# Performance work log

Hardware: AMD Instinct MI355X
Metric: run time of the kernel (lower is better)

Reference implementation:

```python
import jax, jax.numpy as jnp
import numpy as np

B, N, DN, DT = 1024, 200, 128, 128
M = DN + DN + DT  # model_dim = 384 (node + edge + time dims)


def setup_inputs() -> dict:
    key = jax.random.key(0)
    ks = jax.random.split(key, 10)
    rn = lambda k, s, sc=1.0: jax.random.normal(k, s, jnp.float32) * sc
    return {
        'src': rn(ks[0], (B, DN)),
        'src_t': rn(ks[1], (B, 1, DT)),
        'seq': rn(ks[2], (B, N, DN)),
        'seq_t': rn(ks[3], (B, N, DT)),
        'seq_e': rn(ks[4], (B, N, DN)),
        'mask': jax.random.randint(ks[5], (B, N), 0, 2).astype(bool),
        'shared_attn': rn(ks[6], (1, 2 * M), 0.05),
        'fc_w': rn(ks[7], (M, M), 0.05),
        'ln_g': jnp.ones((M,), jnp.float32),
        'ln_b': jnp.zeros((M,), jnp.float32),
        'agg_fc_w1': rn(ks[8], (2 * DN, M + DN), 0.05),
        'agg_fc_w2': rn(ks[9], (DN, 2 * DN), 0.05),
    }


def _layer_norm(x, g, b, eps=1e-5):
    mu = x.mean(-1, keepdims=True)
    var = ((x - mu) ** 2).mean(-1, keepdims=True)
    return (x - mu) * jax.lax.rsqrt(var + eps) * g + b


def reference(src, src_t, seq, seq_t, seq_e, mask, shared_attn, fc_w, ln_g, ln_b, agg_fc_w1, agg_fc_w2):
    # AttnModel.forward with 'simple' Attention (eval mode: dropout off)
    src_ext = src[:, None, :]                                   # [B,1,DN]
    q = jnp.concatenate([src_ext, jnp.zeros_like(src_ext), src_t], axis=2)  # [B,1,M]
    k = jnp.concatenate([seq, seq_e, seq_t], axis=2)            # [B,N,M]
    # F.linear(cat([q_exp, k_exp], -1), shared_attn) == q.w_q + k.w_k (fused, avoids [B,1,N,2M])
    w = shared_attn[0]
    wq, wk = w[:M], w[M:]
    scores = jnp.einsum('bqd,d->bq', q, wq)[:, :, None] + jnp.einsum('bnd,d->bn', k, wk)[:, None, :]  # [B,1,N]
    scores = jnp.where(mask[:, None, :], -1e10, scores)
    attn = jax.nn.softmax(scores, axis=2)                       # [B,1,N]
    out = jnp.einsum('bqn,bnm->bqm', attn, k)                   # [B,1,M] (v == k)
    out = out @ fc_w.T
    out = _layer_norm(out + q, ln_g, ln_b)
    out = out[:, 0, :]                                          # [B,M]
    attn_w = attn[:, 0, :]                                      # [B,N]
    x = jnp.concatenate([out, src], axis=1)                     # [B, M+DN]
    x = jax.nn.relu(x @ agg_fc_w1.T)                            # [B, 2*DN]
    out = x @ agg_fc_w2.T                                       # [B, DN]
    return out, attn_w
```

## Files before the change

### kernel.cpp

```cpp
#include <hip/hip_runtime.h>


constexpr int B_  = 1024;
constexpr int N_  = 200;
constexpr int DN_ = 128;
constexpr int DT_ = 128;
constexpr int M_  = 384;
constexpr int BDIM = 256;
constexpr int NPW  = N_ / 4;

__device__ __forceinline__ float wave_sum(float v) {
#pragma unroll
    for (int off = 32; off > 0; off >>= 1)
        v += __shfl_xor(v, off, 64);
    return v;
}

__global__ __launch_bounds__(BDIM) void tgnn_kernel(
    const float* __restrict__ src,
    const float* __restrict__ src_t,
    const float* __restrict__ seq,
    const float* __restrict__ seq_t,
    const float* __restrict__ seq_e,
    const int*   __restrict__ mask,
    const float* __restrict__ shared_attn,
    const float* __restrict__ fc_w,
    const float* __restrict__ ln_g,
    const float* __restrict__ ln_b,
    const float* __restrict__ w1,
    const float* __restrict__ w2,
    float* __restrict__ out,
    float* __restrict__ attn_out)
{
    const int b    = blockIdx.x;
    const int tid  = threadIdx.x;
    const int wave = tid >> 6;
    const int lane = tid & 63;
    const int e0   = 2 * lane;
    const int e1   = e0 + 1;

    __shared__ float s_p[N_];
    __shared__ float s_q[M_];
    __shared__ float s_oa[4][M_];
    __shared__ float s_outattn[M_];
    __shared__ float s_y[M_ + DN_];
    __shared__ float s_h[2 * DN_];
    __shared__ float s_red[8];

    if (tid < 128) {
        s_q[tid]       = src[b * DN_ + tid];
        s_q[128 + tid] = 0.0f;
        s_q[256 + tid] = src_t[b * DT_ + tid];
    }

    const float* wq = shared_attn;
    const float* wk = shared_attn + M_;
    const float wk0 = wk[e0],       wk1 = wk[e1];
    const float wk2 = wk[128 + e0], wk3 = wk[128 + e1];
    const float wk4 = wk[256 + e0], wk5 = wk[256 + e1];

    float qpart = src[b * DN_ + e0] * wq[e0]
                + src[b * DN_ + e1] * wq[e1]
                + src_t[b * DT_ + e0] * wq[256 + e0]
                + src_t[b * DT_ + e1] * wq[256 + e1];
    const float qdot = wave_sum(qpart);

    float o0 = 0.f, o1 = 0.f, o2 = 0.f, o3 = 0.f, o4 = 0.f, o5 = 0.f;
    float lsum = 0.f;
    const int n_base = wave * NPW;
    for (int n = n_base; n < n_base + NPW; ++n) {
        const long row = (long)(b * N_ + n);
        const float2 a = *(const float2*)&seq  [row * DN_ + e0];
        const float2 e = *(const float2*)&seq_e[row * DN_ + e0];
        const float2 t = *(const float2*)&seq_t[row * DT_ + e0];
        float part = a.x * wk0 + a.y * wk1
                   + e.x * wk2 + e.y * wk3
                   + t.x * wk4 + t.y * wk5;
        float s = wave_sum(part) + qdot;
        float p = mask[row] ? 0.0f : __expf(s);
        if (lane == 0) s_p[n] = p;
        lsum += p;
        o0 += p * a.x; o1 += p * a.y;
        o2 += p * e.x; o3 += p * e.y;
        o4 += p * t.x; o5 += p * t.y;
    }

    if (lane == 0) s_red[wave] = lsum;
    s_oa[wave][e0]       = o0; s_oa[wave][e1]       = o1;
    s_oa[wave][128 + e0] = o2; s_oa[wave][128 + e1] = o3;
    s_oa[wave][256 + e0] = o4; s_oa[wave][256 + e1] = o5;
    __syncthreads();

    const float Z    = s_red[0] + s_red[1] + s_red[2] + s_red[3];
    const float invZ = 1.0f / Z;

    for (int j = tid; j < M_; j += BDIM)
        s_outattn[j] = (s_oa[0][j] + s_oa[1][j] + s_oa[2][j] + s_oa[3][j]) * invZ;
    for (int n = tid; n < N_; n += BDIM)
        attn_out[b * N_ + n] = s_p[n] * invZ;
    __syncthreads();

    for (int r = 0; r < M_ / 4; ++r) {
        const int i = wave * (M_ / 4) + r;
        const float* row = &fc_w[i * M_];
        float part = 0.f;
#pragma unroll
        for (int m = 0; m < 6; ++m)
            part += s_outattn[lane + 64 * m] * row[lane + 64 * m];
        float v = wave_sum(part);
        if (lane == 0) s_y[i] = v + s_q[i];
    }
    __syncthreads();

    float ls = 0.f, lq = 0.f;
    for (int j = tid; j < M_; j += BDIM) {
        float v = s_y[j];
        ls += v; lq += v * v;
    }
    ls = wave_sum(ls); lq = wave_sum(lq);
    if (lane == 0) { s_red[wave] = ls; s_red[4 + wave] = lq; }
    __syncthreads();
    const float mean = (s_red[0] + s_red[1] + s_red[2] + s_red[3]) * (1.0f / M_);
    const float msq  = (s_red[4] + s_red[5] + s_red[6] + s_red[7]) * (1.0f / M_);
    const float rstd = rsqrtf(msq - mean * mean + 1e-5f);
    for (int j = tid; j < M_; j += BDIM)
        s_y[j] = (s_y[j] - mean) * rstd * ln_g[j] + ln_b[j];
    if (tid < 128)
        s_y[M_ + tid] = s_q[tid];
    __syncthreads();

    for (int r = 0; r < 64; ++r) {
        const int i = wave * 64 + r;
        const float* row = &w1[i * (M_ + DN_)];
        float part = 0.f;
#pragma unroll
        for (int m = 0; m < 8; ++m)
            part += s_y[lane + 64 * m] * row[lane + 64 * m];
        float v = wave_sum(part);
        if (lane == 0) s_h[i] = fmaxf(v, 0.0f);
    }
    __syncthreads();

    for (int r = 0; r < 32; ++r) {
        const int i = wave * 32 + r;
        const float* row = &w2[i * (2 * DN_)];
        float part = 0.f;
#pragma unroll
        for (int m = 0; m < 4; ++m)
            part += s_h[lane + 64 * m] * row[lane + 64 * m];
        float v = wave_sum(part);
        if (lane == 0) out[b * DN_ + i] = v;
    }
}

extern "C" void kernel_launch(void* const* d_in, const int* in_sizes, int n_in,
                              void* d_out, int out_size, void* d_ws, size_t ws_size,
                              hipStream_t stream) {
    const float* src         = (const float*)d_in[0];
    const float* src_t       = (const float*)d_in[1];
    const float* seq         = (const float*)d_in[2];
    const float* seq_t       = (const float*)d_in[3];
    const float* seq_e       = (const float*)d_in[4];
    const int*   mask        = (const int*)  d_in[5];
    const float* shared_attn = (const float*)d_in[6];
    const float* fc_w        = (const float*)d_in[7];
    const float* ln_g        = (const float*)d_in[8];
    const float* ln_b        = (const float*)d_in[9];
    const float* w1          = (const float*)d_in[10];
    const float* w2          = (const float*)d_in[11];

    float* out      = (float*)d_out;
    float* attn_out = (float*)d_out + B_ * DN_;

    tgnn_kernel<<<B_, BDIM, 0, stream>>>(src, src_t, seq, seq_t, seq_e, mask,
                                         shared_attn, fc_w, ln_g, ln_b, w1, w2,
                                         out, attn_out);
}
```

Before: 424.0 us.

## Process two batch rows per block, pre-transpose weights, and prefetch keys

A separate kernel now transposes fc_w, w1 and w2 into global buffers each call, so each thread computes one output column with coalesced weight reads instead of one row per wave followed by a shuffle reduction. The main kernel handles two batch rows per 512-thread block, which reuses every weight load across both rows. The key loop moves to float4 loads, with half-waves each handling one key row, and software-prefetches two iterations ahead. The mask is staged in shared memory. The cost is an extra transpose launch per call, higher register pressure and shared-memory use, and half as many blocks.

```diff
diff --git a/kernel.cpp b/kernel.cpp
--- a/kernel.cpp
+++ b/kernel.cpp
@@ -1,22 +1,53 @@
 #include <hip/hip_runtime.h>
 
 
-constexpr int B_  = 1024;
-constexpr int N_  = 200;
-constexpr int DN_ = 128;
-constexpr int DT_ = 128;
-constexpr int M_  = 384;
-constexpr int BDIM = 256;
-constexpr int NPW  = N_ / 4;
-
+constexpr int B_   = 1024;
+constexpr int N_   = 200;
+constexpr int DN_  = 128;
+constexpr int DT_  = 128;
+constexpr int M_   = 384;
+constexpr int BDIM = 512;
+constexpr int ROWS = 2;
+constexpr int WPR  = 4;
+constexpr int NPW  = N_ / WPR;
+constexpr int PAIRS = NPW / 2;
+
+__device__ float g_fcT[M_ * M_];
+__device__ float g_w1T[(M_ + DN_) * (2 * DN_)];
+__device__ float g_w2T[(2 * DN_) * DN_];
+
+__device__ __forceinline__ float half_sum(float v) {
+#pragma unroll
+    for (int off = 16; off > 0; off >>= 1) v += __shfl_xor(v, off, 64);
+    return v;
+}
 __device__ __forceinline__ float wave_sum(float v) {
 #pragma unroll
-    for (int off = 32; off > 0; off >>= 1)
-        v += __shfl_xor(v, off, 64);
+    for (int off = 32; off > 0; off >>= 1) v += __shfl_xor(v, off, 64);
     return v;
 }
 
-__global__ __launch_bounds__(BDIM) void tgnn_kernel(
+struct KP { float4 a, e, t; };
+
+__global__ void transpose_weights(const float* __restrict__ fc_w,
+                                  const float* __restrict__ w1,
+                                  const float* __restrict__ w2) {
+    const int stride = gridDim.x * blockDim.x;
+    for (int idx = blockIdx.x * blockDim.x + threadIdx.x; idx < M_ * M_; idx += stride) {
+        const int j = idx / M_, i = idx - j * M_;
+        g_fcT[idx] = fc_w[i * M_ + j];
+    }
+    for (int idx = blockIdx.x * blockDim.x + threadIdx.x; idx < (M_ + DN_) * (2 * DN_); idx += stride) {
+        const int j = idx >> 8, i = idx & 255;
+        g_w1T[idx] = w1[i * (M_ + DN_) + j];
+    }
+    for (int idx = blockIdx.x * blockDim.x + threadIdx.x; idx < (2 * DN_) * DN_; idx += stride) {
+        const int j = idx >> 7, i = idx & 127;
+        g_w2T[idx] = w2[i * (2 * DN_) + j];
+    }
+}
+
+__global__ __launch_bounds__(BDIM, 4) void tgnn_kernel(
     const float* __restrict__ src,
     const float* __restrict__ src_t,
     const float* __restrict__ seq,
@@ -24,132 +55,177 @@
     const float* __restrict__ seq_e,
     const int*   __restrict__ mask,
     const float* __restrict__ shared_attn,
-    const float* __restrict__ fc_w,
     const float* __restrict__ ln_g,
     const float* __restrict__ ln_b,
-    const float* __restrict__ w1,
-    const float* __restrict__ w2,
     float* __restrict__ out,
     float* __restrict__ attn_out)
 {
-    const int b    = blockIdx.x;
+    const int blk  = blockIdx.x;
     const int tid  = threadIdx.x;
     const int wave = tid >> 6;
     const int lane = tid & 63;
-    const int e0   = 2 * lane;
-    const int e1   = e0 + 1;
-
-    __shared__ float s_p[N_];
-    __shared__ float s_q[M_];
-    __shared__ float s_oa[4][M_];
-    __shared__ float s_outattn[M_];
-    __shared__ float s_y[M_ + DN_];
-    __shared__ float s_h[2 * DN_];
-    __shared__ float s_red[8];
-
-    if (tid < 128) {
-        s_q[tid]       = src[b * DN_ + tid];
-        s_q[128 + tid] = 0.0f;
-        s_q[256 + tid] = src_t[b * DT_ + tid];
+    const int row  = wave >> 2;
+    const int wir  = wave & 3;
+    const int b    = blk * ROWS + row;
+    const int half = lane >> 5;
+    const int sub  = lane & 31;
+    const int c0   = 4 * sub;
+
+    __shared__ float s_p[ROWS][N_];
+    __shared__ float s_q[ROWS][M_];
+    __shared__ float s_oa[8][M_];
+    __shared__ float s_x[ROWS][M_];
+    __shared__ float s_y[ROWS][M_ + DN_];
+    __shared__ float s_h[ROWS][2 * DN_];
+    __shared__ int   s_mask[ROWS][N_];
+    __shared__ float s_red[ROWS][8];
+
+    for (int idx = tid; idx < ROWS * M_; idx += BDIM) {
+        const int r = idx / M_, d = idx - r * M_;
+        const int bb = blk * ROWS + r;
+        float v = (d < DN_) ? src[bb * DN_ + d]
+                            : (d < 2 * DN_ ? 0.0f : src_t[bb * DT_ + (d - 2 * DN_)]);
+        s_q[r][d] = v;
+    }
+    for (int idx = tid; idx < ROWS * N_; idx += BDIM) {
+        const int r = idx / N_, n = idx - r * N_;
+        s_mask[r][n] = mask[(blk * ROWS + r) * N_ + n];
     }
 
     const float* wq = shared_attn;
     const float* wk = shared_attn + M_;
-    const float wk0 = wk[e0],       wk1 = wk[e1];
-    const float wk2 = wk[128 + e0], wk3 = wk[128 + e1];
-    const float wk4 = wk[256 + e0], wk5 = wk[256 + e1];
-
-    float qpart = src[b * DN_ + e0] * wq[e0]
-                + src[b * DN_ + e1] * wq[e1]
-                + src_t[b * DT_ + e0] * wq[256 + e0]
-                + src_t[b * DT_ + e1] * wq[256 + e1];
-    const float qdot = wave_sum(qpart);
-
-    float o0 = 0.f, o1 = 0.f, o2 = 0.f, o3 = 0.f, o4 = 0.f, o5 = 0.f;
+    const float4 wkA = *(const float4*)&wk[c0];
+    const float4 wkE = *(const float4*)&wk[DN_ + c0];
+    const float4 wkT = *(const float4*)&wk[2 * DN_ + c0];
+    const float4 wqA = *(const float4*)&wq[c0];
+    const float4 wqT = *(const float4*)&wq[2 * DN_ + c0];
+
+    __syncthreads();
+
+    const float4 qa = *(const float4*)&s_q[row][c0];
+    const float4 qt = *(const float4*)&s_q[row][2 * DN_ + c0];
+    float qp = qa.x * wqA.x + qa.y * wqA.y + qa.z * wqA.z + qa.w * wqA.w
+             + qt.x * wqT.x + qt.y * wqT.y + qt.z * wqT.z + qt.w * wqT.w;
+    const float qdot = half_sum(qp);
+
+    const long krow0 = (long)b * N_ + wir * NPW + half;
+    const float* pA = seq   + krow0 * DN_ + c0;
+    const float* pE = seq_e + krow0 * DN_ + c0;
+    const float* pT = seq_t + krow0 * DT_ + c0;
+    auto ldp = [&](int it) {
+        KP k;
+        const long off = (long)(2 * it) * DN_;
+        k.a = *(const float4*)(pA + off);
+        k.e = *(const float4*)(pE + off);
+        k.t = *(const float4*)(pT + off);
+        return k;
+    };
+
+    float4 oA = make_float4(0.f, 0.f, 0.f, 0.f);
+    float4 oE = oA, oT = oA;
     float lsum = 0.f;
-    const int n_base = wave * NPW;
-    for (int n = n_base; n < n_base + NPW; ++n) {
-        const long row = (long)(b * N_ + n);
-        const float2 a = *(const float2*)&seq  [row * DN_ + e0];
-        const float2 e = *(const float2*)&seq_e[row * DN_ + e0];
-        const float2 t = *(const float2*)&seq_t[row * DT_ + e0];
-        float part = a.x * wk0 + a.y * wk1
-                   + e.x * wk2 + e.y * wk3
-                   + t.x * wk4 + t.y * wk5;
-        float s = wave_sum(part) + qdot;
-        float p = mask[row] ? 0.0f : __expf(s);
-        if (lane == 0) s_p[n] = p;
-        lsum += p;
-        o0 += p * a.x; o1 += p * a.y;
-        o2 += p * e.x; o3 += p * e.y;
-        o4 += p * t.x; o5 += p * t.y;
-    }
-
-    if (lane == 0) s_red[wave] = lsum;
-    s_oa[wave][e0]       = o0; s_oa[wave][e1]       = o1;
-    s_oa[wave][128 + e0] = o2; s_oa[wave][128 + e1] = o3;
-    s_oa[wave][256 + e0] = o4; s_oa[wave][256 + e1] = o5;
-    __syncthreads();
-
-    const float Z    = s_red[0] + s_red[1] + s_red[2] + s_red[3];
-    const float invZ = 1.0f / Z;
-
-    for (int j = tid; j < M_; j += BDIM)
-        s_outattn[j] = (s_oa[0][j] + s_oa[1][j] + s_oa[2][j] + s_oa[3][j]) * invZ;
-    for (int n = tid; n < N_; n += BDIM)
-        attn_out[b * N_ + n] = s_p[n] * invZ;
-    __syncthreads();
-
-    for (int r = 0; r < M_ / 4; ++r) {
-        const int i = wave * (M_ / 4) + r;
-        const float* row = &fc_w[i * M_];
-        float part = 0.f;
+    KP k0 = ldp(0);
+    KP k1 = ldp(1);
 #pragma unroll
-        for (int m = 0; m < 6; ++m)
-            part += s_outattn[lane + 64 * m] * row[lane + 64 * m];
-        float v = wave_sum(part);
-        if (lane == 0) s_y[i] = v + s_q[i];
-    }
-    __syncthreads();
-
-    float ls = 0.f, lq = 0.f;
-    for (int j = tid; j < M_; j += BDIM) {
-        float v = s_y[j];
-        ls += v; lq += v * v;
-    }
-    ls = wave_sum(ls); lq = wave_sum(lq);
-    if (lane == 0) { s_red[wave] = ls; s_red[4 + wave] = lq; }
-    __syncthreads();
-    const float mean = (s_red[0] + s_red[1] + s_red[2] + s_red[3]) * (1.0f / M_);
-    const float msq  = (s_red[4] + s_red[5] + s_red[6] + s_red[7]) * (1.0f / M_);
-    const float rstd = rsqrtf(msq - mean * mean + 1e-5f);
-    for (int j = tid; j < M_; j += BDIM)
-        s_y[j] = (s_y[j] - mean) * rstd * ln_g[j] + ln_b[j];
-    if (tid < 128)
-        s_y[M_ + tid] = s_q[tid];
-    __syncthreads();
-
-    for (int r = 0; r < 64; ++r) {
-        const int i = wave * 64 + r;
-        const float* row = &w1[i * (M_ + DN_)];
-        float part = 0.f;
-#pragma unroll
-        for (int m = 0; m < 8; ++m)
-            part += s_y[lane + 64 * m] * row[lane + 64 * m];
-        float v = wave_sum(part);
-        if (lane == 0) s_h[i] = fmaxf(v, 0.0f);
-    }
-    __syncthreads();
-
-    for (int r = 0; r < 32; ++r) {
-        const int i = wave * 32 + r;
-        const float* row = &w2[i * (2 * DN_)];
-        float part = 0.f;
-#pragma unroll
-        for (int m = 0; m < 4; ++m)
-            part += s_h[lane + 64 * m] * row[lane + 64 * m];
-        float v = wave_sum(part);
-        if (lane == 0) out[b * DN_ + i] = v;
+    for (int it = 0; it < PAIRS; ++it) {
+        int pf = it + 2; if (pf > PAIRS - 1) pf = PAIRS - 1;
+        KP k2 = ldp(pf);
+
+        float part = k0.a.x * wkA.x + k0.a.y * wkA.y + k0.a.z * wkA.z + k0.a.w * wkA.w
+                   + k0.e.x * wkE.x + k0.e.y * wkE.y + k0.e.z * wkE.z + k0.e.w * wkE.w
+                   + k0.t.x * wkT.x + k0.t.y * wkT.y + k0.t.z * wkT.z + k0.t.w * wkT.w;
+        part = half_sum(part);
+        const int n = wir * NPW + 2 * it + half;
+        const float p = s_mask[row][n] ? 0.0f : __expf(part + qdot);
+        if (sub == 0) { s_p[row][n] = p; lsum += p; }
+        oA.x += p * k0.a.x; oA.y += p * k0.a.y; oA.z += p * k0.a.z; oA.w += p * k0.a.w;
+        oE.x += p * k0.e.x; oE.y += p * k0.e.y; oE.z += p * k0.e.z; oE.w += p * k0.e.w;
+        oT.x += p * k0.t.x; oT.y += p * k0.t.y; oT.z += p * k0.t.z; oT.w += p * k0.t.w;
+        k0 = k1; k1 = k2;
+    }
+
+    oA.x += __shfl_xor(oA.x, 32, 64); oA.y += __shfl_xor(oA.y, 32, 64);
+    oA.z += __shfl_xor(oA.z, 32, 64); oA.w += __shfl_xor(oA.w, 32, 64);
+    oE.x += __shfl_xor(oE.x, 32, 64); oE.y += __shfl_xor(oE.y, 32, 64);
+    oE.z += __shfl_xor(oE.z, 32, 64); oE.w += __shfl_xor(oE.w, 32, 64);
+    oT.x += __shfl_xor(oT.x, 32, 64); oT.y += __shfl_xor(oT.y, 32, 64);
+    oT.z += __shfl_xor(oT.z, 32, 64); oT.w += __shfl_xor(oT.w, 32, 64);
+    lsum += __shfl_xor(lsum, 32, 64);
+    if (lane == 0) s_red[row][wir] = lsum;
+    if (half == 0) {
+        *(float4*)&s_oa[wave][c0]            = oA;
+        *(float4*)&s_oa[wave][DN_ + c0]      = oE;
+        *(float4*)&s_oa[wave][2 * DN_ + c0]  = oT;
+    }
+    __syncthreads();
+
+    for (int idx = tid; idx < ROWS * M_; idx += BDIM) {
+        const int r = idx / M_, d = idx - r * M_;
+        const float Z = s_red[r][0] + s_red[r][1] + s_red[r][2] + s_red[r][3];
+        const float invZ = 1.0f / Z;
+        s_x[r][d] = (s_oa[4 * r + 0][d] + s_oa[4 * r + 1][d] +
+                     s_oa[4 * r + 2][d] + s_oa[4 * r + 3][d]) * invZ;
+    }
+    for (int idx = tid; idx < ROWS * N_; idx += BDIM) {
+        const int r = idx / N_, n = idx - r * N_;
+        const float Z = s_red[r][0] + s_red[r][1] + s_red[r][2] + s_red[r][3];
+        attn_out[(blk * ROWS + r) * N_ + n] = s_p[r][n] * (1.0f / Z);
+    }
+    __syncthreads();
+
+    if (tid < M_) {
+        float acc0 = 0.f, acc1 = 0.f;
+#pragma unroll 8
+        for (int j = 0; j < M_; ++j) {
+            const float w = g_fcT[j * M_ + tid];
+            acc0 += s_x[0][j] * w;
+            acc1 += s_x[1][j] * w;
+        }
+        s_y[0][tid] = acc0 + s_q[0][tid];
+        s_y[1][tid] = acc1 + s_q[1][tid];
+    }
+    __syncthreads();
+
+    {
+        float ls = 0.f, lq = 0.f;
+        for (int j = 64 * wir + lane; j < M_; j += 256) {
+            const float v = s_y[row][j];
+            ls += v; lq += v * v;
+        }
+        ls = wave_sum(ls); lq = wave_sum(lq);
+        if (lane == 0) { s_red[row][wir] = ls; s_red[row][4 + wir] = lq; }
+    }
+    __syncthreads();
+    for (int idx = tid; idx < ROWS * M_; idx += BDIM) {
+        const int r = idx / M_, j = idx - r * M_;
+        const float mean = (s_red[r][0] + s_red[r][1] + s_red[r][2] + s_red[r][3]) * (1.0f / M_);
+        const float msq  = (s_red[r][4] + s_red[r][5] + s_red[r][6] + s_red[r][7]) * (1.0f / M_);
+        const float rstd = rsqrtf(msq - mean * mean + 1e-5f);
+        s_y[r][j] = (s_y[r][j] - mean) * rstd * ln_g[j] + ln_b[j];
+    }
+    for (int idx = tid; idx < ROWS * DN_; idx += BDIM) {
+        const int r = idx >> 7, d = idx & 127;
+        s_y[r][M_ + d] = s_q[r][d];
+    }
+    __syncthreads();
+
+    {
+        const int r = tid >> 8, i = tid & 255;
+        float acc = 0.f;
+#pragma unroll 8
+        for (int j = 0; j < M_ + DN_; ++j)
+            acc += s_y[r][j] * g_w1T[j * 256 + i];
+        s_h[r][i] = fmaxf(acc, 0.0f);
+    }
+    __syncthreads();
+
+    if (tid < 256) {
+        const int r = tid >> 7, i = tid & 127;
+        float acc = 0.f;
+#pragma unroll 8
+        for (int j = 0; j < 2 * DN_; ++j)
+            acc += s_h[r][j] * g_w2T[j * 128 + i];
+        out[(blk * ROWS + r) * DN_ + i] = acc;
     }
 }
 
@@ -169,10 +245,10 @@
     const float* w1          = (const float*)d_in[10];
     const float* w2          = (const float*)d_in[11];
 
-    float* out      = (float*)d_out;
+    float* outp     = (float*)d_out;
     float* attn_out = (float*)d_out + B_ * DN_;
 
-    tgnn_kernel<<<B_, BDIM, 0, stream>>>(src, src_t, seq, seq_t, seq_e, mask,
-                                         shared_attn, fc_w, ln_g, ln_b, w1, w2,
-                                         out, attn_out);
-}
+    transpose_weights<<<256, 256, 0, stream>>>(fc_w, w1, w2);
+    tgnn_kernel<<<B_ / ROWS, BDIM, 0, stream>>>(src, src_t, seq, seq_t, seq_e, mask,
+                                                shared_attn, ln_g, ln_b, outp, attn_out);
+}
```

Result: slower. 491.9 us (+16.0%).
